# Kernel optimization log

Hardware: AMD Instinct MI355X
Metric: run time of the kernel (lower is better)

## Reference

```python
import jax, jax.numpy as jnp
import numpy as np


def setup_inputs() -> dict:
    key = jax.random.key(0)
    k1, k2, k3 = jax.random.split(key, 3)
    B, S, D, N = 2, 2048, 1024, 16
    H = D // N  # head_dim = 64
    x = jax.random.normal(k1, (B, S, D), dtype=jnp.float32)
    W_qkv = jax.random.normal(k2, (N, D, 3 * H), dtype=jnp.float32) / np.sqrt(D).astype(np.float32)
    W_out = jax.random.normal(k3, (N, H, D), dtype=jnp.float32) / np.sqrt(D).astype(np.float32)
    return {"x": x, "W_qkv": W_qkv, "W_out": W_out}


def reference(x, W_qkv, W_out):
    B, S, D = x.shape
    head_dim = W_qkv.shape[-1] // 3
    # QKV projection per head: [B, N, S, 3*H]
    qkv = jnp.einsum('bsd,ndh->bnsh', x, W_qkv)
    q, k, v = jnp.split(qkv, 3, axis=-1)  # each [B, N, S, H]
    scale = jnp.asarray(1.0 / np.sqrt(head_dim), dtype=x.dtype)
    attn = jnp.einsum('bnqh,bnkh->bnqk', q, k) * scale  # [B, N, S, S]
    # causal mask: -1e10 above the diagonal (matches buffer in original)
    mask = jnp.asarray(-1e10, dtype=x.dtype) * (1.0 - jnp.tril(jnp.ones((S, S), dtype=x.dtype)))
    attn = jax.nn.softmax(attn + mask, axis=-1)
    out = jnp.einsum('bnqk,bnkh->bnqh', attn, v)  # [B, N, S, H]
    # faithful to original: raw row-major reshape [B,N,S,H] -> [B, N*H, S]
    out = out.reshape(B, -1, S)
    # faithful to original einsum: d kept, n and h summed over W_out
    return jnp.einsum('bds,nhd->bsd', out, W_out)
```

## Files before the change

kernel.cpp:

```cpp
#include <hip/hip_runtime.h>
#include <hip/hip_bf16.h>

#define B_ 2
#define S_ 2048
#define D_ 1024
#define N_ 16
#define H_ 64

typedef unsigned short u16;
typedef unsigned int u32;
typedef __bf16 bf16x8 __attribute__((ext_vector_type(8)));
typedef u16 u16x8 __attribute__((ext_vector_type(8)));
typedef u32 u32x2 __attribute__((ext_vector_type(2)));
typedef float f4v __attribute__((ext_vector_type(4)));

__device__ __forceinline__ u16 f2b(float f) {
    u32 u = __builtin_bit_cast(u32, f);
    u32 r = (u + 0x7FFFu + ((u >> 16) & 1u)) >> 16;
    return (u16)r;
}
__device__ __forceinline__ bf16x8 asbf(u16x8 v) { return __builtin_bit_cast(bf16x8, v); }
__device__ __forceinline__ u32 cvtpk(float a, float b) {
    u32 r;
    asm("v_cvt_pk_bf16_f32 %0, %1, %2" : "=v"(r) : "v"(a), "v"(b));
    return r;
}
__device__ __forceinline__ void gload16(const u16* g, u16* l) {
    __builtin_amdgcn_global_load_lds((const __attribute__((address_space(1))) void*)g,
                                     (__attribute__((address_space(3))) void*)l, 16, 0, 0);
}

__global__ __launch_bounds__(256) void k_cvt_x(const float* __restrict__ x,
                                               u16* __restrict__ xb) {
    size_t i = ((size_t)blockIdx.x * 256 + threadIdx.x) * 8;
    float4 f0 = *(const float4*)(x + i);
    float4 f1 = *(const float4*)(x + i + 4);
    u16x8 o;
    o[0] = f2b(f0.x); o[1] = f2b(f0.y); o[2] = f2b(f0.z); o[3] = f2b(f0.w);
    o[4] = f2b(f1.x); o[5] = f2b(f1.y); o[6] = f2b(f1.z); o[7] = f2b(f1.w);
    *(u16x8*)(xb + i) = o;
}

__global__ __launch_bounds__(256) void k_cvt_w(const float* __restrict__ w,
                                               u16* __restrict__ wt) {
    __shared__ float T[64][65];
    const int d0 = blockIdx.x * 64, jt = blockIdx.y, n = blockIdx.z;
    const int j0 = jt * 64;
    const float sc = (jt == 0) ? 0.125f * 1.44269504089f : 1.0f;
    const int t = threadIdx.x;
#pragma unroll
    for (int rep = 0; rep < 4; ++rep) {
        int v = t + rep * 256;
        int row = v >> 4, c4 = v & 15;
        float4 f = *(const float4*)(w + ((size_t)(n * 1024 + d0 + row)) * 192 + j0 + c4 * 4);
        T[row][c4 * 4 + 0] = f.x * sc;
        T[row][c4 * 4 + 1] = f.y * sc;
        T[row][c4 * 4 + 2] = f.z * sc;
        T[row][c4 * 4 + 3] = f.w * sc;
    }
    __syncthreads();
#pragma unroll
    for (int rep = 0; rep < 2; ++rep) {
        int c = t + rep * 256;
        int j = c >> 3, db = c & 7;
        u16x8 o;
#pragma unroll
        for (int e = 0; e < 8; ++e) o[e] = f2b(T[db * 8 + e][j]);
        *(u16x8*)(wt + ((size_t)(n * 192 + j0 + j)) * 1024 + d0 + db * 8) = o;
    }
}

__global__ __launch_bounds__(256) void k_wsum(const float* __restrict__ Wout,
                                              float* __restrict__ wsum) {
    __shared__ float red[16][17];
    const int dd = threadIdx.x & 15, rr = threadIdx.x >> 4;
    const int d = blockIdx.x * 16 + dd;
    float s = 0.f;
    for (int r = rr * 64; r < rr * 64 + 64; ++r) s += Wout[(size_t)r * 1024 + d];
    red[rr][dd] = s;
    __syncthreads();
    if (rr == 0) {
        float t = 0.f;
#pragma unroll
        for (int k = 0; k < 16; ++k) t += red[k][dd];
        wsum[d] = t;
    }
}

__global__ __launch_bounds__(512) void k_qkv(const u16* __restrict__ xb,
                                             const u16* __restrict__ wt,
                                             u16* __restrict__ qbuf,
                                             u16* __restrict__ kbuf,
                                             u16* __restrict__ vt) {
    __shared__ u16 As[128 * 64];
    __shared__ u16 Bst[192 * 64];
    const int st = blockIdx.x, n = blockIdx.y;
    const int t = threadIdx.x;
    const int w = t >> 6, lane = t & 63, hi2 = lane >> 4, lo4 = lane & 15;
    const int wm = w >> 2, wn = w & 3;

    const int l8 = lane >> 3, l7 = (lane & 7) * 8;
    const u16* AgL = xb + (size_t)(st * 128 + w * 16 + l8) * 1024 + l7;
    u16* AdL = As + w * 16 * 64;
    const u16* BgL = wt + (size_t)(n * 192 + w * 24 + l8) * 1024 + l7;
    u16* BdL = Bst + w * 24 * 64;

    f4v acc[4][3];
#pragma unroll
    for (int i = 0; i < 4; ++i)
#pragma unroll
        for (int j = 0; j < 3; ++j) acc[i][j] = (f4v){0.f, 0.f, 0.f, 0.f};

    for (int kk = 0; kk < 16; ++kk) {
        __syncthreads();
        const int ko = kk * 64;
        gload16(AgL + ko, AdL);
        gload16(AgL + ko + (size_t)8 * 1024, AdL + 8 * 64);
        gload16(BgL + ko, BdL);
        gload16(BgL + ko + (size_t)8 * 1024, BdL + 8 * 64);
        gload16(BgL + ko + (size_t)16 * 1024, BdL + 16 * 64);
        __syncthreads();
        bf16x8 fa[4][2];
#pragma unroll
        for (int ms = 0; ms < 4; ++ms) {
            const u16* ar = As + (wm * 64 + ms * 16 + lo4) * 64;
            fa[ms][0] = asbf(*(const u16x8*)(ar + hi2 * 8));
            fa[ms][1] = asbf(*(const u16x8*)(ar + hi2 * 8 + 32));
        }
        __builtin_amdgcn_s_setprio(1);
#pragma unroll
        for (int fj = 0; fj < 3; ++fj) {
            const u16* br = Bst + (wn * 48 + fj * 16 + lo4) * 64;
            bf16x8 fb0 = asbf(*(const u16x8*)(br + hi2 * 8));
            bf16x8 fb1 = asbf(*(const u16x8*)(br + hi2 * 8 + 32));
#pragma unroll
            for (int ms = 0; ms < 4; ++ms) {
                acc[ms][fj] = __builtin_amdgcn_mfma_f32_16x16x32_bf16(fa[ms][0], fb0, acc[ms][fj], 0, 0, 0);
                acc[ms][fj] = __builtin_amdgcn_mfma_f32_16x16x32_bf16(fa[ms][1], fb1, acc[ms][fj], 0, 0, 0);
            }
        }
        __builtin_amdgcn_s_setprio(0);
    }

    const int b = st >> 4, s128 = (st & 15) * 128;
    u16* Cs = As;
#pragma unroll
    for (int sec = 0; sec < 3; ++sec) {
        __syncthreads();
#pragma unroll
        for (int fj = 0; fj < 3; ++fj) {
            const int base = wn * 48 + fj * 16;
            if ((base >> 6) == sec) {
                const int col = base - sec * 64 + lo4;
#pragma unroll
                for (int ms = 0; ms < 4; ++ms)
#pragma unroll
                    for (int r = 0; r < 4; ++r)
                        Cs[(wm * 64 + ms * 16 + hi2 * 4 + r) * 64 + col] = f2b(acc[ms][fj][r]);
            }
        }
        __syncthreads();
        if (sec == 2) {
            const int h = t & 63, sb = t >> 6;
            u16x8 o0, o1;
#pragma unroll
            for (int e = 0; e < 8; ++e) o0[e] = Cs[(sb * 16 + e) * 64 + h];
#pragma unroll
            for (int e = 0; e < 8; ++e) o1[e] = Cs[(sb * 16 + 8 + e) * 64 + h];
            u16* dst = vt + ((size_t)(b * 16 + n) * 64 + h) * 2048 + s128 + sb * 16;
            *(u16x8*)dst = o0;
            *(u16x8*)(dst + 8) = o1;
        } else {
            const int row = t >> 2, off = (t & 3) * 16;
            u16* dst = (sec == 0) ? qbuf : kbuf;
            dst += ((size_t)(b * 16 + n) * 2048 + s128 + row) * 64 + off;
            *(u16x8*)dst = *(const u16x8*)(Cs + row * 64 + off);
            *(u16x8*)(dst + 8) = *(const u16x8*)(Cs + row * 64 + off + 8);
        }
    }
}

__global__ __launch_bounds__(512) void k_attn(const u16* __restrict__ qbuf,
                                              const u16* __restrict__ kbuf,
                                              const u16* __restrict__ vt,
                                              const float* __restrict__ wsum,
                                              float* __restrict__ out) {
    __shared__ u16 SMEM[16384];
    u16* Ks = SMEM;
    u16* Vs = SMEM + 4096;
    u16* Ps = SMEM + 8192;
    const int id = blockIdx.x;
    const int bn = id & 31;
    const int qx = id >> 5;
    const int qb = (qx < 8) ? (15 - 2 * qx) : (2 * (qx - 8));
    const int t = threadIdx.x;
    const int w = t >> 6, lane = t & 63, hi2 = lane >> 4, lo4 = lane & 15;

    const int q = qb * 128 + w * 16 + lo4;
    const u16* Qp = qbuf + ((size_t)bn * 2048 + q) * 64;
    bf16x8 bq0 = asbf(*(const u16x8*)(Qp + hi2 * 8));
    bf16x8 bq1 = asbf(*(const u16x8*)(Qp + 32 + hi2 * 8));

    const int srow = t >> 3, so = t & 7;
    const u16* Kg = kbuf + (size_t)bn * 2048 * 64 + (size_t)srow * 64 + so * 8;
    const u16* Vg = vt + (size_t)bn * 64 * 2048 + (size_t)srow * 2048 + so * 8;
    u16* Kl = Ks + srow * 64 + ((so * 8) ^ ((srow & 7) << 3));
    u16* Vl = Vs + srow * 64 + ((so * 8) ^ ((srow & 7) << 3));

    f4v accO[4];
#pragma unroll
    for (int i = 0; i < 4; ++i) accO[i] = (f4v){0.f, 0.f, 0.f, 0.f};
    float m = -3.0e38f, l = 0.f;

    const int rsw = (lo4 & 7) << 3;
    u16* Pw = Ps + w * 1024 + lo4 * 64;
    const int nkb = 2 * qb + 2;

    u16x8 kreg = *(const u16x8*)(Kg);
    u16x8 vreg = *(const u16x8*)(Vg);

    for (int kb = 0; kb < nkb; ++kb) {
        __syncthreads();
        *(u16x8*)Kl = kreg;
        *(u16x8*)Vl = vreg;
        if (kb + 1 < nkb) {
            kreg = *(const u16x8*)(Kg + (size_t)(kb + 1) * 4096);
            vreg = *(const u16x8*)(Vg + (kb + 1) * 64);
        }
        __syncthreads();

        f4v s4[4];
#pragma unroll
        for (int i = 0; i < 4; ++i) s4[i] = (f4v){0.f, 0.f, 0.f, 0.f};
        __builtin_amdgcn_s_setprio(1);
#pragma unroll
        for (int fi = 0; fi < 4; ++fi) {
            const u16* kr = Ks + (fi * 16 + lo4) * 64;
            bf16x8 ka0 = asbf(*(const u16x8*)(kr + ((hi2 * 8) ^ rsw)));
            bf16x8 ka1 = asbf(*(const u16x8*)(kr + ((hi2 * 8 + 32) ^ rsw)));
            s4[fi] = __builtin_amdgcn_mfma_f32_16x16x32_bf16(ka0, bq0, s4[fi], 0, 0, 0);
            s4[fi] = __builtin_amdgcn_mfma_f32_16x16x32_bf16(ka1, bq1, s4[fi], 0, 0, 0);
        }
        __builtin_amdgcn_s_setprio(0);

        if (kb >= 2 * qb) {
#pragma unroll
            for (int fi = 0; fi < 4; ++fi)
#pragma unroll
                for (int r = 0; r < 4; ++r) {
                    int kvg = kb * 64 + fi * 16 + hi2 * 4 + r;
                    if (kvg > q) s4[fi][r] = -3.0e38f;
                }
        }

        float pm = s4[0][0];
#pragma unroll
        for (int fi = 0; fi < 4; ++fi)
#pragma unroll
            for (int r = 0; r < 4; ++r) pm = fmaxf(pm, s4[fi][r]);
        pm = fmaxf(pm, __shfl_xor(pm, 16));
        pm = fmaxf(pm, __shfl_xor(pm, 32));

        if (__any(pm > m + 8.0f)) {
            float mn = fmaxf(m, pm);
            float fs = __builtin_exp2f(m - mn);
            m = mn;
            l *= fs;
#pragma unroll
            for (int fh = 0; fh < 4; ++fh)
#pragma unroll
                for (int r = 0; r < 4; ++r) accO[fh][r] *= fs;
        }
        float ts = 0.f;
#pragma unroll
        for (int fi = 0; fi < 4; ++fi) {
#pragma unroll
            for (int r = 0; r < 4; ++r) {
                float pv = __builtin_exp2f(s4[fi][r] - m);
                s4[fi][r] = pv;
                ts += pv;
            }
            u32x2 pk;
            pk[0] = cvtpk(s4[fi][0], s4[fi][1]);
            pk[1] = cvtpk(s4[fi][2], s4[fi][3]);
            *(u32x2*)(Pw + ((fi * 16 + hi2 * 4) ^ rsw)) = pk;
        }
        ts += __shfl_xor(ts, 16);
        ts += __shfl_xor(ts, 32);
        l += ts;

        bf16x8 pb0 = asbf(*(const u16x8*)(Pw + ((hi2 * 8) ^ rsw)));
        bf16x8 pb1 = asbf(*(const u16x8*)(Pw + ((32 + hi2 * 8) ^ rsw)));
        __builtin_amdgcn_s_setprio(1);
#pragma unroll
        for (int fh = 0; fh < 4; ++fh) {
            const u16* vr = Vs + (fh * 16 + lo4) * 64;
            bf16x8 va0 = asbf(*(const u16x8*)(vr + ((hi2 * 8) ^ rsw)));
            bf16x8 va1 = asbf(*(const u16x8*)(vr + ((hi2 * 8 + 32) ^ rsw)));
            accO[fh] = __builtin_amdgcn_mfma_f32_16x16x32_bf16(va0, pb0, accO[fh], 0, 0, 0);
            accO[fh] = __builtin_amdgcn_mfma_f32_16x16x32_bf16(va1, pb1, accO[fh], 0, 0, 0);
        }
        __builtin_amdgcn_s_setprio(0);
    }

    __syncthreads();
    float* Osh = (float*)SMEM;
    {
        float inv = 1.f / l;
        const int orl = w * 16 + lo4;
        const int osw = (lo4 & 7) << 2;
        float* Or = Osh + orl * 64;
#pragma unroll
        for (int fh = 0; fh < 4; ++fh) {
            f4v o;
#pragma unroll
            for (int r = 0; r < 4; ++r) o[r] = accO[fh][r] * inv;
            *(f4v*)(Or + ((fh * 16 + hi2 * 4) ^ osw)) = o;
        }
    }
    __syncthreads();
    {
        const int b = bn >> 4, n = bn & 15;
        const int d0 = n * 64 + qb * 4;
        float4 wv = *(const float4*)(wsum + d0);
#pragma unroll
        for (int rep = 0; rep < 4; ++rep) {
            int p = rep * 512 + t;
            int h = p & 63, tt = p >> 6;
            const int key = (tt & 7) << 2;
            const int hc = h ^ key;
            float4 o;
            o.x = Osh[(tt)*64 + hc] * wv.x;
            o.y = Osh[(32 + tt) * 64 + hc] * wv.y;
            o.z = Osh[(64 + tt) * 64 + hc] * wv.z;
            o.w = Osh[(96 + tt) * 64 + hc] * wv.w;
            *(float4*)(out + ((size_t)b * 2048 + p) * 1024 + d0) = o;
        }
    }
}

extern "C" void kernel_launch(void* const* d_in, const int* in_sizes, int n_in,
                              void* d_out, int out_size, void* d_ws, size_t ws_size,
                              hipStream_t stream) {
    const float* x = (const float*)d_in[0];
    const float* Wqkv = (const float*)d_in[1];
    const float* Wout = (const float*)d_in[2];
    float* out = (float*)d_out;

    char* p = (char*)d_ws;
    float* wsum = (float*)p; p += 4096;
    u16* xb = (u16*)p; p += (size_t)4096 * 1024 * 2;
    u16* wt = (u16*)p; p += (size_t)16 * 192 * 1024 * 2;
    u16* qb_ = (u16*)p; p += (size_t)32 * 2048 * 64 * 2;
    u16* kb_ = (u16*)p; p += (size_t)32 * 2048 * 64 * 2;
    u16* vt_ = (u16*)p; p += (size_t)32 * 2048 * 64 * 2;

    k_cvt_x<<<2048, 256, 0, stream>>>(x, xb);
    k_cvt_w<<<dim3(16, 3, 16), 256, 0, stream>>>(Wqkv, wt);
    k_wsum<<<64, 256, 0, stream>>>(Wout, wsum);
    k_qkv<<<dim3(32, 16), 512, 0, stream>>>(xb, wt, qb_, kb_, vt_);
    k_attn<<<512, 512, 0, stream>>>(qb_, kb_, vt_, wsum, out);
}
```

Measured before the change: 99.52 us.

## Load K/V MFMA fragments directly from global memory, drop LDS staging and barriers

Removes the shared-memory staging of K and V tiles and both per-iteration __syncthreads. Each wave now loads its MFMA operand fragments for K and V straight from global memory into registers, relying on L1/L2 to serve the reuse across the 8 waves. Launch bounds add a min-blocks hint of 4 to push occupancy. The cost is 8x redundant global/L1 traffic per block and exposed load latency without explicit prefetch. The V loads are also strided by 2048 elements per row.

New measurement: 182.4 us. +83.2%, slower.

```diff
diff --git a/kernel.cpp b/kernel.cpp
--- a/kernel.cpp
+++ b/kernel.cpp
@@ -180,15 +180,13 @@
     }
 }
 
-__global__ __launch_bounds__(512) void k_attn(const u16* __restrict__ qbuf,
-                                              const u16* __restrict__ kbuf,
-                                              const u16* __restrict__ vt,
-                                              const float* __restrict__ wsum,
-                                              float* __restrict__ out) {
+__global__ __launch_bounds__(512, 4) void k_attn(const u16* __restrict__ qbuf,
+                                                 const u16* __restrict__ kbuf,
+                                                 const u16* __restrict__ vt,
+                                                 const float* __restrict__ wsum,
+                                                 float* __restrict__ out) {
     __shared__ u16 SMEM[16384];
-    u16* Ks = SMEM;
-    u16* Vs = SMEM + 4096;
-    u16* Ps = SMEM + 8192;
+    u16* Ps = SMEM;
     const int id = blockIdx.x;
     const int bn = id & 31;
     const int qx = id >> 5;
@@ -201,11 +199,8 @@
     bf16x8 bq0 = asbf(*(const u16x8*)(Qp + hi2 * 8));
     bf16x8 bq1 = asbf(*(const u16x8*)(Qp + 32 + hi2 * 8));
 
-    const int srow = t >> 3, so = t & 7;
-    const u16* Kg = kbuf + (size_t)bn * 2048 * 64 + (size_t)srow * 64 + so * 8;
-    const u16* Vg = vt + (size_t)bn * 64 * 2048 + (size_t)srow * 2048 + so * 8;
-    u16* Kl = Ks + srow * 64 + ((so * 8) ^ ((srow & 7) << 3));
-    u16* Vl = Vs + srow * 64 + ((so * 8) ^ ((srow & 7) << 3));
+    const u16* Kfrag = kbuf + (size_t)bn * 2048 * 64 + (size_t)lo4 * 64 + hi2 * 8;
+    const u16* Vfrag = vt + (size_t)bn * 64 * 2048 + (size_t)lo4 * 2048 + hi2 * 8;
 
     f4v accO[4];
 #pragma unroll
@@ -216,32 +211,32 @@
     u16* Pw = Ps + w * 1024 + lo4 * 64;
     const int nkb = 2 * qb + 2;
 
-    u16x8 kreg = *(const u16x8*)(Kg);
-    u16x8 vreg = *(const u16x8*)(Vg);
-
     for (int kb = 0; kb < nkb; ++kb) {
-        __syncthreads();
-        *(u16x8*)Kl = kreg;
-        *(u16x8*)Vl = vreg;
-        if (kb + 1 < nkb) {
-            kreg = *(const u16x8*)(Kg + (size_t)(kb + 1) * 4096);
-            vreg = *(const u16x8*)(Vg + (kb + 1) * 64);
-        }
-        __syncthreads();
-
+        const u16* Kt = Kfrag + (size_t)kb * 64 * 64;
+        u16x8 kf[4][2];
+#pragma unroll
+        for (int fi = 0; fi < 4; ++fi) {
+            kf[fi][0] = *(const u16x8*)(Kt + fi * 16 * 64);
+            kf[fi][1] = *(const u16x8*)(Kt + fi * 16 * 64 + 32);
+        }
         f4v s4[4];
 #pragma unroll
         for (int i = 0; i < 4; ++i) s4[i] = (f4v){0.f, 0.f, 0.f, 0.f};
         __builtin_amdgcn_s_setprio(1);
 #pragma unroll
         for (int fi = 0; fi < 4; ++fi) {
-            const u16* kr = Ks + (fi * 16 + lo4) * 64;
-            bf16x8 ka0 = asbf(*(const u16x8*)(kr + ((hi2 * 8) ^ rsw)));
-            bf16x8 ka1 = asbf(*(const u16x8*)(kr + ((hi2 * 8 + 32) ^ rsw)));
-            s4[fi] = __builtin_amdgcn_mfma_f32_16x16x32_bf16(ka0, bq0, s4[fi], 0, 0, 0);
-            s4[fi] = __builtin_amdgcn_mfma_f32_16x16x32_bf16(ka1, bq1, s4[fi], 0, 0, 0);
+            s4[fi] = __builtin_amdgcn_mfma_f32_16x16x32_bf16(asbf(kf[fi][0]), bq0, s4[fi], 0, 0, 0);
+            s4[fi] = __builtin_amdgcn_mfma_f32_16x16x32_bf16(asbf(kf[fi][1]), bq1, s4[fi], 0, 0, 0);
         }
         __builtin_amdgcn_s_setprio(0);
+
+        const u16* Vt2 = Vfrag + kb * 64;
+        u16x8 vf[4][2];
+#pragma unroll
+        for (int fh = 0; fh < 4; ++fh) {
+            vf[fh][0] = *(const u16x8*)(Vt2 + (size_t)fh * 16 * 2048);
+            vf[fh][1] = *(const u16x8*)(Vt2 + (size_t)fh * 16 * 2048 + 32);
+        }
 
         if (kb >= 2 * qb) {
 #pragma unroll
@@ -294,11 +289,8 @@
         __builtin_amdgcn_s_setprio(1);
 #pragma unroll
         for (int fh = 0; fh < 4; ++fh) {
-            const u16* vr = Vs + (fh * 16 + lo4) * 64;
-            bf16x8 va0 = asbf(*(const u16x8*)(vr + ((hi2 * 8) ^ rsw)));
-            bf16x8 va1 = asbf(*(const u16x8*)(vr + ((hi2 * 8 + 32) ^ rsw)));
-            accO[fh] = __builtin_amdgcn_mfma_f32_16x16x32_bf16(va0, pb0, accO[fh], 0, 0, 0);
-            accO[fh] = __builtin_amdgcn_mfma_f32_16x16x32_bf16(va1, pb1, accO[fh], 0, 0, 0);
+            accO[fh] = __builtin_amdgcn_mfma_f32_16x16x32_bf16(asbf(vf[fh][0]), pb0, accO[fh], 0, 0, 0);
+            accO[fh] = __builtin_amdgcn_mfma_f32_16x16x32_bf16(asbf(vf[fh][1]), pb1, accO[fh], 0, 0, 0);
         }
         __builtin_amdgcn_s_setprio(0);
     }
```
